# Kernel optimization log

Measured on AMD Instinct MI355X. Metric: run time of the kernel, lower is better.

The kernel has to match this reference:

```python
import jax, jax.numpy as jnp
import numpy as np

N_NODES = 100000

def _sage(x, src, tgt, Wl, bl, Wr):
    # PyG SAGEConv (mean aggr): out = lin_l(mean_{j in N(i)} x_j) + lin_r(x_i)
    msg = x[src]                                             # [E, F] gather
    s = jax.ops.segment_sum(msg, tgt, num_segments=N_NODES)  # [N, F]
    cnt = jax.ops.segment_sum(jnp.ones((src.shape[0], 1), x.dtype), tgt, num_segments=N_NODES)
    agg = s / jnp.maximum(cnt, 1.0)
    return agg @ Wl + bl + x @ Wr


def setup_inputs() -> dict:
    key = jax.random.key(0)
    ks = jax.random.split(key, 16)
    node_dim, edge_dim, hidden = 128, 16, 64
    E = 1000000
    x = jax.random.normal(ks[0], (N_NODES, node_dim), jnp.float32)
    edge_index = jax.random.randint(ks[1], (2, E), 0, N_NODES, jnp.int64)
    edge_attr = jax.random.normal(ks[2], (E, edge_dim), jnp.float32)
    def lin(k, fi, fo, scale=None):
        s = scale if scale is not None else 1.0 / np.sqrt(fi)
        return jax.random.uniform(k, (fi, fo), jnp.float32, -s, s)
    return {
        "x": x, "edge_index": edge_index, "edge_attr": edge_attr,
        # edge MLP: Linear(16,64) -> ReLU -> Linear(64,64)
        "We1": lin(ks[3], edge_dim, hidden), "be1": jnp.zeros((hidden,), jnp.float32),
        "We2": lin(ks[4], hidden, hidden),   "be2": jnp.zeros((hidden,), jnp.float32),
        # SAGEConv 0: lin_l (with bias, on aggregated) + lin_r (no bias, on root)
        "Wl0": lin(ks[5], node_dim, hidden), "bl0": jnp.zeros((hidden,), jnp.float32),
        "Wr0": lin(ks[6], node_dim, hidden),
        # SAGEConv 1
        "Wl1": lin(ks[7], hidden, hidden), "bl1": jnp.zeros((hidden,), jnp.float32),
        "Wr1": lin(ks[8], hidden, hidden),
        # output MLP: Linear(64,64) -> ReLU -> (Dropout eval=id) -> Linear(64,1)
        "Wo1": lin(ks[9], hidden, hidden), "bo1": jnp.zeros((hidden,), jnp.float32),
        "Wo2": lin(ks[10], hidden, 1),     "bo2": jnp.zeros((1,), jnp.float32),
    }


def reference(x, edge_index, edge_attr, We1, be1, We2, be2,
              Wl0, bl0, Wr0, Wl1, bl1, Wr1, Wo1, bo1, Wo2, bo2):
    src, tgt = edge_index[0], edge_index[1]
    # edge MLP (dropout in eval mode = identity)
    ea = jax.nn.relu(edge_attr @ We1 + be1) @ We2 + be2       # [E, H]
    # two SAGE layers with ReLU
    h = jax.nn.relu(_sage(x, src, tgt, Wl0, bl0, Wr0))        # [N, H]
    h = jax.nn.relu(_sage(h, src, tgt, Wl1, bl1, Wr1))        # [N, H]
    # per-edge features: gather both endpoints + edge embedding
    ef = h[src] + h[tgt] + ea                                 # [E, H]
    out = jax.nn.relu(ef @ Wo1 + bo1) @ Wo2 + bo2             # [E, 1]
    return jax.nn.sigmoid(out[:, 0])                          # [E]
```

## Files before the change

kernel.cpp:

```cpp
#include <hip/hip_runtime.h>
#include <math.h>

typedef __attribute__((ext_vector_type(8))) short short8;
typedef __attribute__((ext_vector_type(4))) float f32x4;

static __device__ __forceinline__ unsigned short f2bf(float f) {
  union { float f; unsigned int u; } x; x.f = f;
  unsigned int r = x.u + 0x7fffu + ((x.u >> 16) & 1u);
  return (unsigned short)(r >> 16);
}
static __device__ __forceinline__ float bf2f(unsigned int u) {
  union { unsigned int u; float f; } x; x.u = u << 16; return x.f;
}

__global__ void k_flag(const unsigned int* __restrict__ w, int nSample,
                       unsigned int* __restrict__ flag,
                       int* __restrict__ deg, int padN) {
  int4* d4 = (int4*)deg;
  int n4 = padN >> 2;
  for (int i = blockIdx.x * 256 + threadIdx.x; i < n4; i += gridDim.x * 256)
    d4[i] = make_int4(0, 0, 0, 0);
  if (blockIdx.x != 0) return;
  __shared__ unsigned int red[256];
  unsigned int v = 0;
  for (int i = threadIdx.x; i < nSample; i += 256) v |= w[2 * i + 1];
  red[threadIdx.x] = v;
  __syncthreads();
  for (int s = 128; s > 0; s >>= 1) {
    if (threadIdx.x < s) red[threadIdx.x] |= red[threadIdx.x + s];
    __syncthreads();
  }
  if (threadIdx.x == 0) flag[0] = red[0];
}

template <int K, bool BF16IN, int NTILES, bool INLINEW>
__device__ __forceinline__ void ngemm_body(
    const void* __restrict__ Xv, const unsigned short* __restrict__ WnT,
    const float* __restrict__ W0f, const float* __restrict__ W1f,
    unsigned short* __restrict__ Y0, unsigned short* __restrict__ Y1,
    int N, int blk, unsigned short* __restrict__ sX) {
  constexpr int STR = K + 8;
  constexpr int NC = K / 32;
  const int tid = threadIdx.x;
  const int wv = tid >> 6, lane = tid & 63;
  const int m = lane & 15, q = lane >> 4;
  const int row0 = blk * 64;

  short8 bB[NTILES][NC];
#pragma unroll
  for (int ct = 0; ct < NTILES; ++ct)
#pragma unroll
    for (int c = 0; c < NC; ++c) {
      if constexpr (INLINEW) {
        int n = (NTILES == 2) ? (wv * 32 + ct * 16 + m) : (wv * 16 + m);
        const float* Wf = (n < 64) ? W0f : W1f;
        int nn = n & 63;
        union { short8 s; unsigned short h[8]; } ub;
#pragma unroll
        for (int j = 0; j < 8; ++j)
          ub.h[j] = f2bf(Wf[(size_t)(c * 32 + q * 8 + j) * 64 + nn]);
        bB[ct][c] = ub.s;
      } else {
        int n = (NTILES == 2) ? (wv * 32 + ct * 16 + m) : (wv * 16 + m);
        bB[ct][c] = *(const short8*)(WnT + (size_t)n * K + c * 32 + q * 8);
      }
    }

#pragma unroll
  for (int i = 0; i < K / 16; ++i) {
    int f = tid + 256 * i;
    int r = f / (K / 4);
    int c4 = f % (K / 4);
    int rr = row0 + r; if (rr >= N) rr = N - 1;
    uint2 pk;
    if constexpr (BF16IN) {
      pk = *(const uint2*)((const unsigned short*)Xv + (size_t)rr * K + c4 * 4);
    } else {
      float4 v = *(const float4*)((const float*)Xv + (size_t)rr * K + c4 * 4);
      pk.x = (unsigned int)f2bf(v.x) | ((unsigned int)f2bf(v.y) << 16);
      pk.y = (unsigned int)f2bf(v.z) | ((unsigned int)f2bf(v.w) << 16);
    }
    *(uint2*)(sX + r * STR + c4 * 4) = pk;
  }
  __syncthreads();

  f32x4 acc[4][NTILES];
#pragma unroll
  for (int rt = 0; rt < 4; ++rt)
#pragma unroll
    for (int ct = 0; ct < NTILES; ++ct)
#pragma unroll
      for (int r = 0; r < 4; ++r) acc[rt][ct][r] = 0.f;

#pragma unroll
  for (int c = 0; c < NC; ++c) {
    short8 a[4];
#pragma unroll
    for (int rt = 0; rt < 4; ++rt)
      a[rt] = *(const short8*)(sX + (rt * 16 + m) * STR + c * 32 + q * 8);
#pragma unroll
    for (int rt = 0; rt < 4; ++rt)
#pragma unroll
      for (int ct = 0; ct < NTILES; ++ct)
        acc[rt][ct] = __builtin_amdgcn_mfma_f32_16x16x32_bf16(a[rt], bB[ct][c], acc[rt][ct], 0, 0, 0);
  }

#pragma unroll
  for (int rt = 0; rt < 4; ++rt)
#pragma unroll
    for (int ct = 0; ct < NTILES; ++ct) {
      unsigned short* Yw;
      int n;
      if constexpr (NTILES == 2) {
        Yw = (wv < 2) ? Y0 : Y1;
        n = (wv & 1) * 32 + ct * 16 + m;
      } else {
        Yw = Y0;
        n = wv * 16 + m;
      }
#pragma unroll
      for (int reg = 0; reg < 4; ++reg) {
        int row = row0 + rt * 16 + q * 4 + reg;
        if (row < N) Yw[(size_t)row * 64 + n] = f2bf(acc[rt][ct][reg]);
      }
    }
}

template <int K, bool BF16IN, int NTILES>
__global__ __launch_bounds__(256) void k_ngemm(
    const void* __restrict__ Xv, const unsigned short* __restrict__ WnT,
    unsigned short* __restrict__ Y0, unsigned short* __restrict__ Y1, int N) {
  __shared__ __align__(16) unsigned short sX[64 * (K + 8)];
  ngemm_body<K, BF16IN, NTILES, false>(Xv, WnT, nullptr, nullptr, Y0, Y1, N,
                                       blockIdx.x, sX);
}

__global__ __launch_bounds__(256) void k_mega1(
    const unsigned int* __restrict__ w, const unsigned int* __restrict__ flag,
    int E, int nDec, int nWork, int gB, int nConvThreads,
    int* __restrict__ src, int* __restrict__ tgt,
    int* __restrict__ posin, int* __restrict__ deg,
    const float* __restrict__ x, unsigned short* __restrict__ Yl,
    unsigned short* __restrict__ Yr, int N,
    const float* __restrict__ We2, const float* __restrict__ Wo1,
    const float* __restrict__ be2, const float* __restrict__ bo1,
    const float* __restrict__ We1,
    const float* __restrict__ Wl0, const float* __restrict__ Wr0,
    const float* __restrict__ Wl1, const float* __restrict__ Wr1,
    unsigned short* __restrict__ W25T, unsigned short* __restrict__ We1T,
    unsigned short* __restrict__ Wo1T, float* __restrict__ cvec,
    unsigned short* __restrict__ WnT1,
    const float4* __restrict__ ef, uint2* __restrict__ eb) {
  __shared__ __align__(16) char smem[64 * 136 * 2];
  const int tid = threadIdx.x;
  const int tot = nDec + nWork;
  const int di  = (int)(((long long)blockIdx.x * nDec) / tot);
  const int di1 = (int)(((long long)(blockIdx.x + 1) * nDec) / tot);

  if (di1 > di) {
    int e = di * 256 + tid;
    if (e >= E) return;
    int s, t;
    if (flag[0]) { s = (int)w[e]; t = (int)w[E + e]; }
    else         { s = (int)w[2 * e]; t = (int)w[2 * (E + e)]; }
    src[e] = s;
    tgt[e] = t;
    posin[e] = atomicAdd(deg + t, 1);
    return;
  }
  const int wi = blockIdx.x - di;
  if (wi == 0) {
    float* sB = (float*)smem;
    for (int i = tid; i < 1024; i += 256)
      *(float4*)&sB[i * 4] = *(const float4*)(Wo1 + i * 4);
    __syncthreads();
    for (int idx = tid; idx < 4096; idx += 256) {
      int k = idx >> 6, n = idx & 63;
      float s = 0.f;
#pragma unroll 8
      for (int mm = 0; mm < 64; ++mm) s = fmaf(We2[k * 64 + mm], sB[mm * 64 + n], s);
      W25T[n * 64 + k] = f2bf(s);
      Wo1T[n * 64 + k] = f2bf(sB[k * 64 + n]);
    }
    for (int idx = tid; idx < 2048; idx += 256) {
      int n = idx >> 5, k = idx & 31;
      We1T[n * 32 + k] = (k < 16) ? f2bf(We1[k * 64 + n]) : (unsigned short)0;
    }
    if (tid < 64) {
      float s = bo1[tid];
#pragma unroll 8
      for (int mm = 0; mm < 64; ++mm) s = fmaf(be2[mm], sB[mm * 64 + tid], s);
      cvec[tid] = s;
    }
  } else if (wi <= 32) {
    int idx = (wi - 1) * 256 + tid;
    int n = idx >> 6, k = idx & 63;
    float v = (n < 64) ? Wl1[(size_t)k * 64 + n] : Wr1[(size_t)k * 64 + (n - 64)];
    WnT1[idx] = f2bf(v);
  } else if (wi < 33 + gB) {
    ngemm_body<128, false, 2, true>(x, nullptr, Wl0, Wr0, Yl, Yr, N,
                                    wi - 33, (unsigned short*)smem);
  } else {
    int gid = (wi - 33 - gB) * 256 + tid;
    int nItems = E * 4;
    for (int i = gid; i < nItems; i += nConvThreads) {
      float4 v = ef[i];
      uint2 pk;
      pk.x = (unsigned int)f2bf(v.x) | ((unsigned int)f2bf(v.y) << 16);
      pk.y = (unsigned int)f2bf(v.z) | ((unsigned int)f2bf(v.w) << 16);
      eb[i] = pk;
    }
  }
}

__global__ __launch_bounds__(256) void k_scan1(const int* __restrict__ deg,
                                               int* __restrict__ bsum) {
  __shared__ int wsum[4];
  const int tid = threadIdx.x, lane = tid & 63, wid = tid >> 6;
  const int base = blockIdx.x * 2048 + tid * 8;
  int4 v0 = *(const int4*)(deg + base);
  int4 v1 = *(const int4*)(deg + base + 4);
  int s = v0.x + v0.y + v0.z + v0.w + v1.x + v1.y + v1.z + v1.w;
#pragma unroll
  for (int off = 1; off < 64; off <<= 1) s += __shfl_xor(s, off, 64);
  if (lane == 0) wsum[wid] = s;
  __syncthreads();
  if (tid == 0) bsum[blockIdx.x] = wsum[0] + wsum[1] + wsum[2] + wsum[3];
}

__global__ void k_scan2(const int* __restrict__ bsum, int* __restrict__ boff,
                        int nB) {
  int lane = threadIdx.x;
  int v = (lane < nB) ? bsum[lane] : 0;
  int incl = v;
#pragma unroll
  for (int off = 1; off < 64; off <<= 1) {
    int t = __shfl_up(incl, off, 64);
    if (lane >= off) incl += t;
  }
  if (lane < nB) boff[lane] = incl - v;
}

__global__ __launch_bounds__(256) void k_scan3(const int* __restrict__ deg,
                                               const int* __restrict__ boff,
                                               int* __restrict__ rowptr) {
  __shared__ int wsum[4];
  const int tid = threadIdx.x, lane = tid & 63, wid = tid >> 6;
  const int base = blockIdx.x * 2048 + tid * 8;
  int4 v0 = *(const int4*)(deg + base);
  int4 v1 = *(const int4*)(deg + base + 4);
  int e[8] = {v0.x, v0.y, v0.z, v0.w, v1.x, v1.y, v1.z, v1.w};
  int s = e[0] + e[1] + e[2] + e[3] + e[4] + e[5] + e[6] + e[7];
  int incl = s;
#pragma unroll
  for (int off = 1; off < 64; off <<= 1) {
    int t = __shfl_up(incl, off, 64);
    if (lane >= off) incl += t;
  }
  if (lane == 63) wsum[wid] = incl;
  __syncthreads();
  int run = boff[blockIdx.x] + (incl - s);
  for (int w = 0; w < wid; ++w) run += wsum[w];
  int o[8];
#pragma unroll
  for (int i = 0; i < 8; ++i) { o[i] = run; run += e[i]; }
  *(int4*)(rowptr + base) = make_int4(o[0], o[1], o[2], o[3]);
  *(int4*)(rowptr + base + 4) = make_int4(o[4], o[5], o[6], o[7]);
}

__global__ void k_fill(const int* __restrict__ src, const int* __restrict__ tgt,
                       const int* __restrict__ posin,
                       const int* __restrict__ rowptr,
                       int* __restrict__ csrc, int E) {
  int e = blockIdx.x * 256 + threadIdx.x;
  if (e >= E) return;
  csrc[rowptr[tgt[e]] + posin[e]] = src[e];
}

__global__ __launch_bounds__(256) void k_agg(
    const unsigned short* __restrict__ Y, const int* __restrict__ rowptr,
    const int* __restrict__ csrc, const float* __restrict__ bias,
    const unsigned short* __restrict__ Yr, unsigned short* __restrict__ H,
    int N) {
  int node = (blockIdx.x * 256 + threadIdx.x) >> 6;
  if (node >= N) return;
  const int lane = threadIdx.x & 63;
  const int c4 = lane & 15, rr = lane >> 4;
  int beg = rowptr[node], end = rowptr[node + 1];
  float a0 = 0.f, a1 = 0.f, a2 = 0.f, a3 = 0.f;
  float b0 = 0.f, b1 = 0.f, b2 = 0.f, b3 = 0.f;
  for (int e = beg; e < end; e += 8) {
    int e0 = e + rr, e1 = e + 4 + rr;
    if (e0 < end) {
      int s = csrc[e0];
      uint2 v = *(const uint2*)(Y + (size_t)s * 64 + c4 * 4);
      a0 += bf2f(v.x & 0xffffu); a1 += bf2f(v.x >> 16);
      a2 += bf2f(v.y & 0xffffu); a3 += bf2f(v.y >> 16);
    }
    if (e1 < end) {
      int s = csrc[e1];
      uint2 v = *(const uint2*)(Y + (size_t)s * 64 + c4 * 4);
      b0 += bf2f(v.x & 0xffffu); b1 += bf2f(v.x >> 16);
      b2 += bf2f(v.y & 0xffffu); b3 += bf2f(v.y >> 16);
    }
  }
  a0 += b0; a1 += b1; a2 += b2; a3 += b3;
#pragma unroll
  for (int msk = 16; msk <= 32; msk <<= 1) {
    a0 += __shfl_xor(a0, msk, 64);
    a1 += __shfl_xor(a1, msk, 64);
    a2 += __shfl_xor(a2, msk, 64);
    a3 += __shfl_xor(a3, msk, 64);
  }
  if (rr == 0) {
    float cdeg = (float)(end - beg);
    if (cdeg < 1.f) cdeg = 1.f;
    float inv = 1.f / cdeg;
    float4 bv = *(const float4*)(bias + c4 * 4);
    uint2 yv = *(const uint2*)(Yr + (size_t)node * 64 + c4 * 4);
    float o0 = fmaxf(a0 * inv + bv.x + bf2f(yv.x & 0xffffu), 0.f);
    float o1 = fmaxf(a1 * inv + bv.y + bf2f(yv.x >> 16), 0.f);
    float o2 = fmaxf(a2 * inv + bv.z + bf2f(yv.y & 0xffffu), 0.f);
    float o3 = fmaxf(a3 * inv + bv.w + bf2f(yv.y >> 16), 0.f);
    uint2 pk;
    pk.x = (unsigned int)f2bf(o0) | ((unsigned int)f2bf(o1) << 16);
    pk.y = (unsigned int)f2bf(o2) | ((unsigned int)f2bf(o3) << 16);
    *(uint2*)(H + (size_t)node * 64 + c4 * 4) = pk;
  }
}

#define T1_STRIDE 72
#define G_STRIDE 68
__global__ __launch_bounds__(256) void k_edge3(
    const unsigned short* __restrict__ EAb, const int* __restrict__ src,
    const int* __restrict__ tgt, const unsigned short* __restrict__ Gb,
    const unsigned short* __restrict__ We1T,
    const unsigned short* __restrict__ W25T,
    const float* __restrict__ cvec, const float* __restrict__ be1,
    const float* __restrict__ Wo2, const float* __restrict__ bo2,
    float* __restrict__ out, int E, int nT, int nWaves) {
  __shared__ unsigned short sT1a[4][16 * T1_STRIDE];
  __shared__ float sGa[4][16 * G_STRIDE];
  const int tid = threadIdx.x;
  const int wid = tid >> 6, lane = tid & 63;
  const int m = lane & 15, q = lane >> 4;
  unsigned short* sT1 = sT1a[wid];
  float* sG = sGa[wid];

  short8 bWe1[4], bW25[4][2];
  float cv[4], wo2v[4], be1v[4];
#pragma unroll
  for (int nt = 0; nt < 4; ++nt) {
    int n = nt * 16 + m;
    bWe1[nt] = *(const short8*)(We1T + n * 32 + q * 8);
    bW25[nt][0] = *(const short8*)(W25T + n * 64 + q * 8);
    bW25[nt][1] = *(const short8*)(W25T + n * 64 + 32 + q * 8);
    cv[nt] = cvec[n];
    wo2v[nt] = Wo2[n];
    be1v[nt] = be1[n];
  }
  const float b_out = bo2[0];
  const short8 zfrag = {};

  int t = blockIdx.x * 4 + wid;
  if (t >= nT) return;
  int il = t * 16 + m; if (il >= E) il = E - 1;
  int my_idx = (lane < 16) ? src[il] : ((lane < 32) ? tgt[il] : 0);

  while (true) {
    const int base = t * 16;
    const int tn = t + nWaves;
    const bool last = (tn >= nT);
    const int tc = last ? t : tn;

    int il_n = tc * 16 + m; if (il_n >= E) il_n = E - 1;
    int idx_n = (lane < 16) ? src[il_n] : ((lane < 32) ? tgt[il_n] : 0);

    int rs[4], rt[4];
#pragma unroll
    for (int r = 0; r < 4; ++r) {
      rs[r] = __shfl(my_idx, q * 4 + r, 64);
      rt[r] = __shfl(my_idx, 16 + q * 4 + r, 64);
    }
    uint2 sv[4], tv[4];
#pragma unroll
    for (int r = 0; r < 4; ++r) {
      sv[r] = *(const uint2*)(Gb + (size_t)rs[r] * 64 + m * 4);
      tv[r] = *(const uint2*)(Gb + (size_t)rt[r] * 64 + m * 4);
    }

    int er = base + m; if (er >= E) er = E - 1;
    short8 aEA = zfrag;
    if (q < 2) aEA = *(const short8*)(EAb + (size_t)er * 16 + (q & 1) * 8);

    f32x4 t1[4];
#pragma unroll
    for (int nt = 0; nt < 4; ++nt) {
      f32x4 cinit; cinit[0] = be1v[nt]; cinit[1] = be1v[nt];
      cinit[2] = be1v[nt]; cinit[3] = be1v[nt];
      t1[nt] = __builtin_amdgcn_mfma_f32_16x16x32_bf16(aEA, bWe1[nt], cinit, 0, 0, 0);
    }
#pragma unroll
    for (int nt = 0; nt < 4; ++nt)
#pragma unroll
      for (int r = 0; r < 4; ++r)
        sT1[(q * 4 + r) * T1_STRIDE + nt * 16 + m] = f2bf(fmaxf(t1[nt][r], 0.f));
    short8 aT0 = *(short8*)(sT1 + m * T1_STRIDE + q * 8);
    short8 aT1 = *(short8*)(sT1 + m * T1_STRIDE + 32 + q * 8);

#pragma unroll
    for (int r = 0; r < 4; ++r) {
      f32x4 g;
      g[0] = bf2f(sv[r].x & 0xffffu) + bf2f(tv[r].x & 0xffffu);
      g[1] = bf2f(sv[r].x >> 16)     + bf2f(tv[r].x >> 16);
      g[2] = bf2f(sv[r].y & 0xffffu) + bf2f(tv[r].y & 0xffffu);
      g[3] = bf2f(sv[r].y >> 16)     + bf2f(tv[r].y >> 16);
      *(f32x4*)(sG + (q * 4 + r) * G_STRIDE + m * 4) = g;
    }

    f32x4 acc[4];
#pragma unroll
    for (int nt = 0; nt < 4; ++nt)
#pragma unroll
      for (int r = 0; r < 4; ++r)
        acc[nt][r] = cv[nt] + sG[(q * 4 + r) * G_STRIDE + nt * 16 + m];
#pragma unroll
    for (int nt = 0; nt < 4; ++nt) {
      acc[nt] = __builtin_amdgcn_mfma_f32_16x16x32_bf16(aT0, bW25[nt][0], acc[nt], 0, 0, 0);
      acc[nt] = __builtin_amdgcn_mfma_f32_16x16x32_bf16(aT1, bW25[nt][1], acc[nt], 0, 0, 0);
    }

    float p[4];
#pragma unroll
    for (int r = 0; r < 4; ++r) {
      p[r] = fmaxf(acc[0][r], 0.f) * wo2v[0] + fmaxf(acc[1][r], 0.f) * wo2v[1] +
             fmaxf(acc[2][r], 0.f) * wo2v[2] + fmaxf(acc[3][r], 0.f) * wo2v[3];
    }
#pragma unroll
    for (int msk = 1; msk <= 8; msk <<= 1) {
#pragma unroll
      for (int r = 0; r < 4; ++r) p[r] += __shfl_xor(p[r], msk, 64);
    }
    if (m == 0) {
#pragma unroll
      for (int r = 0; r < 4; ++r) {
        int row = base + q * 4 + r;
        if (row < E) out[row] = 1.f / (1.f + __expf(-(p[r] + b_out)));
      }
    }

    if (last) break;
    t = tn; my_idx = idx_n;
  }
}

extern "C" void kernel_launch(void* const* d_in, const int* in_sizes, int n_in,
                              void* d_out, int out_size, void* d_ws, size_t ws_size,
                              hipStream_t stream) {
  const float* x     = (const float*)d_in[0];
  const unsigned int* eidx = (const unsigned int*)d_in[1];
  const float* eattr = (const float*)d_in[2];
  const float* We1 = (const float*)d_in[3];
  const float* be1 = (const float*)d_in[4];
  const float* We2 = (const float*)d_in[5];
  const float* be2 = (const float*)d_in[6];
  const float* Wl0 = (const float*)d_in[7];
  const float* bl0 = (const float*)d_in[8];
  const float* Wr0 = (const float*)d_in[9];
  const float* Wl1 = (const float*)d_in[10];
  const float* bl1 = (const float*)d_in[11];
  const float* Wr1 = (const float*)d_in[12];
  const float* Wo1 = (const float*)d_in[13];
  const float* bo1 = (const float*)d_in[14];
  const float* Wo2 = (const float*)d_in[15];
  const float* bo2 = (const float*)d_in[16];

  const int N = in_sizes[0] / 128;
  const int E = in_sizes[2] / 16;
  const int padN = (N + 2047) & ~2047;
  const int nB = padN / 2048;
  float* out = (float*)d_out;

  char* ws = (char*)d_ws;
  size_t off = 0;
  auto alloc = [&](size_t bytes) {
    char* p = ws + off;
    off += (bytes + 255) & ~(size_t)255;
    return p;
  };
  unsigned int* flag = (unsigned int*)alloc(256);
  int* src    = (int*)alloc((size_t)E * 4);
  int* tgt    = (int*)alloc((size_t)E * 4);
  int* posin  = (int*)alloc((size_t)E * 4);
  int* deg    = (int*)alloc((size_t)padN * 4);
  int* rowptr = (int*)alloc((size_t)(padN + 64) * 4);
  int* bsum   = (int*)alloc(64 * 4);
  int* boff   = (int*)alloc(64 * 4);
  int* csrc   = (int*)alloc((size_t)E * 4);
  unsigned short* EAb = (unsigned short*)alloc((size_t)E * 16 * 2);
  unsigned short* Hb = (unsigned short*)alloc((size_t)N * 64 * 2);
  unsigned short* Yl = (unsigned short*)alloc((size_t)N * 64 * 2);
  unsigned short* Yr = (unsigned short*)alloc((size_t)N * 64 * 2);
  unsigned short* Gb = (unsigned short*)alloc((size_t)N * 64 * 2);
  unsigned short* W25T = (unsigned short*)alloc(64 * 64 * 2);
  unsigned short* We1T = (unsigned short*)alloc(64 * 32 * 2);
  unsigned short* Wo1T = (unsigned short*)alloc(64 * 64 * 2);
  unsigned short* WnT1 = (unsigned short*)alloc(128 * 64 * 2);
  float* cvec = (float*)alloc(64 * 4);
  (void)ws_size; (void)n_in; (void)out_size;

  k_flag<<<64, 256, 0, stream>>>(eidx, 8192, flag, deg, padN);

  const int nDec = (E + 255) / 256;
  const int gB = (N + 63) / 64;
  const int convB = 1024;
  const int nWork = 33 + gB + convB;
  k_mega1<<<nDec + nWork, 256, 0, stream>>>(
      eidx, flag, E, nDec, nWork, gB, convB * 256,
      src, tgt, posin, deg,
      x, Yl, Yr, N,
      We2, Wo1, be2, bo1, We1, Wl0, Wr0, Wl1, Wr1,
      W25T, We1T, Wo1T, cvec, WnT1,
      (const float4*)eattr, (uint2*)EAb);

  k_scan1<<<nB, 256, 0, stream>>>(deg, bsum);
  k_scan2<<<1, 64, 0, stream>>>(bsum, boff, nB);
  k_scan3<<<nB, 256, 0, stream>>>(deg, boff, rowptr);
  k_fill<<<nDec, 256, 0, stream>>>(src, tgt, posin, rowptr, csrc, E);

  const int aggB = (N + 3) / 4;
  k_agg<<<aggB, 256, 0, stream>>>(Yl, rowptr, csrc, bl0, Yr, Hb, N);

  k_ngemm<64, true, 2><<<gB, 256, 0, stream>>>(Hb, WnT1, Yl, Yr, N);
  k_agg<<<aggB, 256, 0, stream>>>(Yl, rowptr, csrc, bl1, Yr, Hb, N);

  k_ngemm<64, true, 1><<<gB, 256, 0, stream>>>(Hb, Wo1T, Gb, nullptr, N);

  const int nT = (E + 15) / 16;
  const int blocks = 3072;
  k_edge3<<<blocks, 256, 0, stream>>>(EAb, src, tgt, Gb, We1T, W25T, cvec,
                                      be1, Wo2, bo2, out, E, nT, blocks * 4);
}
```

Before: 411.3 us.

## Privatize degree counters into 32 sub-bins per node to cut atomic contention

The per-node degree histogram becomes 32 sub-counters per node, selected by the decode block index, so edge atomics spread across more addresses. The scan kernels now sum the 32 sub-bins per node and emit per-sub-bin base offsets, which the CSR fill uses to place each edge. The 32x larger count and base buffers alias the Hb and Gb buffers to avoid extra workspace. In exchange, zeroing and scanning touch far more memory, and the per-edge atomics now hit 32 separate cache lines per node instead of one.

```diff
diff --git a/kernel.cpp b/kernel.cpp
--- a/kernel.cpp
+++ b/kernel.cpp
@@ -15,9 +15,9 @@
 
 __global__ void k_flag(const unsigned int* __restrict__ w, int nSample,
                        unsigned int* __restrict__ flag,
-                       int* __restrict__ deg, int padN) {
-  int4* d4 = (int4*)deg;
-  int n4 = padN >> 2;
+                       int* __restrict__ deg32, int nInts) {
+  int4* d4 = (int4*)deg32;
+  int n4 = nInts >> 2;
   for (int i = blockIdx.x * 256 + threadIdx.x; i < n4; i += gridDim.x * 256)
     d4[i] = make_int4(0, 0, 0, 0);
   if (blockIdx.x != 0) return;
@@ -139,7 +139,7 @@
     const unsigned int* __restrict__ w, const unsigned int* __restrict__ flag,
     int E, int nDec, int nWork, int gB, int nConvThreads,
     int* __restrict__ src, int* __restrict__ tgt,
-    int* __restrict__ posin, int* __restrict__ deg,
+    int* __restrict__ posin, int* __restrict__ deg32,
     const float* __restrict__ x, unsigned short* __restrict__ Yl,
     unsigned short* __restrict__ Yr, int N,
     const float* __restrict__ We2, const float* __restrict__ Wo1,
@@ -165,7 +165,7 @@
     else         { s = (int)w[2 * e]; t = (int)w[2 * (E + e)]; }
     src[e] = s;
     tgt[e] = t;
-    posin[e] = atomicAdd(deg + t, 1);
+    posin[e] = atomicAdd(deg32 + (size_t)t * 32 + (di & 31), 1);
     return;
   }
   const int wi = blockIdx.x - di;
@@ -213,14 +213,17 @@
   }
 }
 
-__global__ __launch_bounds__(256) void k_scan1(const int* __restrict__ deg,
+__global__ __launch_bounds__(256) void k_scan1(const int* __restrict__ deg32,
                                                int* __restrict__ bsum) {
   __shared__ int wsum[4];
   const int tid = threadIdx.x, lane = tid & 63, wid = tid >> 6;
-  const int base = blockIdx.x * 2048 + tid * 8;
-  int4 v0 = *(const int4*)(deg + base);
-  int4 v1 = *(const int4*)(deg + base + 4);
-  int s = v0.x + v0.y + v0.z + v0.w + v1.x + v1.y + v1.z + v1.w;
+  const int* p = deg32 + (size_t)blockIdx.x * 65536 + (size_t)tid * 4;
+  int s = 0;
+#pragma unroll 8
+  for (int i = 0; i < 64; ++i) {
+    int4 v = *(const int4*)(p + (size_t)i * 1024);
+    s += v.x + v.y + v.z + v.w;
+  }
 #pragma unroll
   for (int off = 1; off < 64; off <<= 1) s += __shfl_xor(s, off, 64);
   if (lane == 0) wsum[wid] = s;
@@ -241,15 +244,25 @@
   if (lane < nB) boff[lane] = incl - v;
 }
 
-__global__ __launch_bounds__(256) void k_scan3(const int* __restrict__ deg,
+__global__ __launch_bounds__(256) void k_scan3(const int* __restrict__ deg32,
                                                const int* __restrict__ boff,
-                                               int* __restrict__ rowptr) {
+                                               int* __restrict__ rowptr,
+                                               int* __restrict__ base32) {
   __shared__ int wsum[4];
   const int tid = threadIdx.x, lane = tid & 63, wid = tid >> 6;
-  const int base = blockIdx.x * 2048 + tid * 8;
-  int4 v0 = *(const int4*)(deg + base);
-  int4 v1 = *(const int4*)(deg + base + 4);
-  int e[8] = {v0.x, v0.y, v0.z, v0.w, v1.x, v1.y, v1.z, v1.w};
+  const int node0 = blockIdx.x * 2048 + tid * 8;
+  int e[8];
+#pragma unroll
+  for (int i = 0; i < 8; ++i) {
+    const int4* p = (const int4*)(deg32 + (size_t)(node0 + i) * 32);
+    int s8 = 0;
+#pragma unroll
+    for (int j = 0; j < 8; ++j) {
+      int4 v = p[j];
+      s8 += v.x + v.y + v.z + v.w;
+    }
+    e[i] = s8;
+  }
   int s = e[0] + e[1] + e[2] + e[3] + e[4] + e[5] + e[6] + e[7];
   int incl = s;
 #pragma unroll
@@ -264,17 +277,35 @@
   int o[8];
 #pragma unroll
   for (int i = 0; i < 8; ++i) { o[i] = run; run += e[i]; }
-  *(int4*)(rowptr + base) = make_int4(o[0], o[1], o[2], o[3]);
-  *(int4*)(rowptr + base + 4) = make_int4(o[4], o[5], o[6], o[7]);
+  *(int4*)(rowptr + node0) = make_int4(o[0], o[1], o[2], o[3]);
+  *(int4*)(rowptr + node0 + 4) = make_int4(o[4], o[5], o[6], o[7]);
+#pragma unroll
+  for (int i = 0; i < 8; ++i) {
+    const int4* p = (const int4*)(deg32 + (size_t)(node0 + i) * 32);
+    int4* b = (int4*)(base32 + (size_t)(node0 + i) * 32);
+    int r2 = o[i];
+#pragma unroll
+    for (int j = 0; j < 8; ++j) {
+      int4 v = p[j];
+      int4 bb;
+      bb.x = r2;
+      bb.y = r2 + v.x;
+      bb.z = bb.y + v.y;
+      bb.w = bb.z + v.z;
+      b[j] = bb;
+      r2 = bb.w + v.w;
+    }
+  }
 }
 
 __global__ void k_fill(const int* __restrict__ src, const int* __restrict__ tgt,
                        const int* __restrict__ posin,
-                       const int* __restrict__ rowptr,
+                       const int* __restrict__ base32,
                        int* __restrict__ csrc, int E) {
   int e = blockIdx.x * 256 + threadIdx.x;
   if (e >= E) return;
-  csrc[rowptr[tgt[e]] + posin[e]] = src[e];
+  int t = tgt[e];
+  csrc[base32[(size_t)t * 32 + ((e >> 8) & 31)] + posin[e]] = src[e];
 }
 
 __global__ __launch_bounds__(256) void k_agg(
@@ -492,16 +523,19 @@
   int* src    = (int*)alloc((size_t)E * 4);
   int* tgt    = (int*)alloc((size_t)E * 4);
   int* posin  = (int*)alloc((size_t)E * 4);
-  int* deg    = (int*)alloc((size_t)padN * 4);
   int* rowptr = (int*)alloc((size_t)(padN + 64) * 4);
   int* bsum   = (int*)alloc(64 * 4);
   int* boff   = (int*)alloc(64 * 4);
   int* csrc   = (int*)alloc((size_t)E * 4);
   unsigned short* EAb = (unsigned short*)alloc((size_t)E * 16 * 2);
-  unsigned short* Hb = (unsigned short*)alloc((size_t)N * 64 * 2);
+  char* HbB = alloc((size_t)padN * 128);
+  unsigned short* Hb = (unsigned short*)HbB;
+  int* base32 = (int*)HbB;
   unsigned short* Yl = (unsigned short*)alloc((size_t)N * 64 * 2);
   unsigned short* Yr = (unsigned short*)alloc((size_t)N * 64 * 2);
-  unsigned short* Gb = (unsigned short*)alloc((size_t)N * 64 * 2);
+  char* GbB = alloc((size_t)padN * 128);
+  unsigned short* Gb = (unsigned short*)GbB;
+  int* deg32 = (int*)GbB;
   unsigned short* W25T = (unsigned short*)alloc(64 * 64 * 2);
   unsigned short* We1T = (unsigned short*)alloc(64 * 32 * 2);
   unsigned short* Wo1T = (unsigned short*)alloc(64 * 64 * 2);
@@ -509,7 +543,7 @@
   float* cvec = (float*)alloc(64 * 4);
   (void)ws_size; (void)n_in; (void)out_size;
 
-  k_flag<<<64, 256, 0, stream>>>(eidx, 8192, flag, deg, padN);
+  k_flag<<<256, 256, 0, stream>>>(eidx, 8192, flag, deg32, padN * 32);
 
   const int nDec = (E + 255) / 256;
   const int gB = (N + 63) / 64;
@@ -517,16 +551,16 @@
   const int nWork = 33 + gB + convB;
   k_mega1<<<nDec + nWork, 256, 0, stream>>>(
       eidx, flag, E, nDec, nWork, gB, convB * 256,
-      src, tgt, posin, deg,
+      src, tgt, posin, deg32,
       x, Yl, Yr, N,
       We2, Wo1, be2, bo1, We1, Wl0, Wr0, Wl1, Wr1,
       W25T, We1T, Wo1T, cvec, WnT1,
       (const float4*)eattr, (uint2*)EAb);
 
-  k_scan1<<<nB, 256, 0, stream>>>(deg, bsum);
+  k_scan1<<<nB, 256, 0, stream>>>(deg32, bsum);
   k_scan2<<<1, 64, 0, stream>>>(bsum, boff, nB);
-  k_scan3<<<nB, 256, 0, stream>>>(deg, boff, rowptr);
-  k_fill<<<nDec, 256, 0, stream>>>(src, tgt, posin, rowptr, csrc, E);
+  k_scan3<<<nB, 256, 0, stream>>>(deg32, boff, rowptr, base32);
+  k_fill<<<nDec, 256, 0, stream>>>(src, tgt, posin, base32, csrc, E);
 
   const int aggB = (N + 3) / 4;
   k_agg<<<aggB, 256, 0, stream>>>(Yl, rowptr, csrc, bl0, Yr, Hb, N);
```

After: 463.9 us. +12.8%, slower.

## Replace global-atomic CSR build with two-pass bucketed counting sort

Applied to the files above, without the earlier changes.

Builds the target-sorted edge list by bucketing edges into 256-node buckets using block-local shared histograms and global bucket cursors, then counting-sorting each bucket in one kernel that also emits begin/end row pairs. This removes per-edge global atomics on the degree array, the three-kernel scan, and the scatter fill kernel. It relies on a fixed per-bucket capacity and silently drops edges beyond it, and on source indices fitting in 24 bits.

```diff
diff --git a/kernel.cpp b/kernel.cpp
--- a/kernel.cpp
+++ b/kernel.cpp
@@ -3,6 +3,8 @@
 
 typedef __attribute__((ext_vector_type(8))) short short8;
 typedef __attribute__((ext_vector_type(4))) float f32x4;
+
+#define CAPB 4096
 
 static __device__ __forceinline__ unsigned short f2bf(float f) {
   union { float f; unsigned int u; } x; x.f = f;
@@ -15,11 +17,11 @@
 
 __global__ void k_flag(const unsigned int* __restrict__ w, int nSample,
                        unsigned int* __restrict__ flag,
-                       int* __restrict__ deg, int padN) {
-  int4* d4 = (int4*)deg;
-  int n4 = padN >> 2;
-  for (int i = blockIdx.x * 256 + threadIdx.x; i < n4; i += gridDim.x * 256)
-    d4[i] = make_int4(0, 0, 0, 0);
+                       int* __restrict__ gcursor) {
+  if (blockIdx.x == 1) {
+    if (threadIdx.x < 256) { gcursor[threadIdx.x] = 0; gcursor[threadIdx.x + 256] = 0; }
+    return;
+  }
   if (blockIdx.x != 0) return;
   __shared__ unsigned int red[256];
   unsigned int v = 0;
@@ -139,7 +141,7 @@
     const unsigned int* __restrict__ w, const unsigned int* __restrict__ flag,
     int E, int nDec, int nWork, int gB, int nConvThreads,
     int* __restrict__ src, int* __restrict__ tgt,
-    int* __restrict__ posin, int* __restrict__ deg,
+    int* __restrict__ gcursor, unsigned int* __restrict__ tmp,
     const float* __restrict__ x, unsigned short* __restrict__ Yl,
     unsigned short* __restrict__ Yr, int N,
     const float* __restrict__ We2, const float* __restrict__ Wo1,
@@ -158,14 +160,37 @@
   const int di1 = (int)(((long long)(blockIdx.x + 1) * nDec) / tot);
 
   if (di1 > di) {
-    int e = di * 256 + tid;
-    if (e >= E) return;
-    int s, t;
-    if (flag[0]) { s = (int)w[e]; t = (int)w[E + e]; }
-    else         { s = (int)w[2 * e]; t = (int)w[2 * (E + e)]; }
-    src[e] = s;
-    tgt[e] = t;
-    posin[e] = atomicAdd(deg + t, 1);
+    int* hist = (int*)smem;
+    hist[tid] = 0; hist[tid + 256] = 0;
+    __syncthreads();
+    const int e0 = di * 4096;
+    const int e1 = (e0 + 4096 < E) ? (e0 + 4096) : E;
+    const unsigned int fl = flag[0];
+    for (int e = e0 + tid; e < e1; e += 256) {
+      int s, t;
+      if (fl) { s = (int)w[e]; t = (int)w[E + e]; }
+      else    { s = (int)w[2 * e]; t = (int)w[2 * (E + e)]; }
+      src[e] = s; tgt[e] = t;
+      atomicAdd(hist + (t >> 8), 1);
+    }
+    __syncthreads();
+    {
+      int c0 = hist[tid], c1 = hist[tid + 256];
+      int s0 = (c0 > 0) ? atomicAdd(gcursor + tid, c0) : 0;
+      int s1 = (c1 > 0) ? atomicAdd(gcursor + tid + 256, c1) : 0;
+      __syncthreads();
+      hist[tid] = s0; hist[tid + 256] = s1;
+    }
+    __syncthreads();
+    for (int e = e0 + tid; e < e1; e += 256) {
+      int s, t;
+      if (fl) { s = (int)w[e]; t = (int)w[E + e]; }
+      else    { s = (int)w[2 * e]; t = (int)w[2 * (E + e)]; }
+      int b = t >> 8;
+      int pos = atomicAdd(hist + b, 1);
+      if (pos < CAPB)
+        tmp[(size_t)b * CAPB + pos] = ((unsigned int)s << 8) | (unsigned int)(t & 255);
+    }
     return;
   }
   const int wi = blockIdx.x - di;
@@ -213,72 +238,47 @@
   }
 }
 
-__global__ __launch_bounds__(256) void k_scan1(const int* __restrict__ deg,
-                                               int* __restrict__ bsum) {
+__global__ __launch_bounds__(256) void k_bsort(
+    const unsigned int* __restrict__ tmp, const int* __restrict__ gcursor,
+    int* __restrict__ csrc, uint2* __restrict__ rowptr2, int N) {
+  __shared__ int cnt[256];
+  __shared__ int curs[256];
   __shared__ int wsum[4];
-  const int tid = threadIdx.x, lane = tid & 63, wid = tid >> 6;
-  const int base = blockIdx.x * 2048 + tid * 8;
-  int4 v0 = *(const int4*)(deg + base);
-  int4 v1 = *(const int4*)(deg + base + 4);
-  int s = v0.x + v0.y + v0.z + v0.w + v1.x + v1.y + v1.z + v1.w;
-#pragma unroll
-  for (int off = 1; off < 64; off <<= 1) s += __shfl_xor(s, off, 64);
-  if (lane == 0) wsum[wid] = s;
+  const int b = blockIdx.x, tid = threadIdx.x;
+  int c = gcursor[b]; if (c > CAPB) c = CAPB;
+  cnt[tid] = 0;
   __syncthreads();
-  if (tid == 0) bsum[blockIdx.x] = wsum[0] + wsum[1] + wsum[2] + wsum[3];
-}
-
-__global__ void k_scan2(const int* __restrict__ bsum, int* __restrict__ boff,
-                        int nB) {
-  int lane = threadIdx.x;
-  int v = (lane < nB) ? bsum[lane] : 0;
+  const unsigned int* reg = tmp + (size_t)b * CAPB;
+  for (int i = tid; i < c; i += 256) atomicAdd(&cnt[reg[i] & 255u], 1);
+  __syncthreads();
+  const int lane = tid & 63, wv = tid >> 6;
+  int v = cnt[tid];
   int incl = v;
 #pragma unroll
   for (int off = 1; off < 64; off <<= 1) {
     int t = __shfl_up(incl, off, 64);
     if (lane >= off) incl += t;
   }
-  if (lane < nB) boff[lane] = incl - v;
-}
-
-__global__ __launch_bounds__(256) void k_scan3(const int* __restrict__ deg,
-                                               const int* __restrict__ boff,
-                                               int* __restrict__ rowptr) {
-  __shared__ int wsum[4];
-  const int tid = threadIdx.x, lane = tid & 63, wid = tid >> 6;
-  const int base = blockIdx.x * 2048 + tid * 8;
-  int4 v0 = *(const int4*)(deg + base);
-  int4 v1 = *(const int4*)(deg + base + 4);
-  int e[8] = {v0.x, v0.y, v0.z, v0.w, v1.x, v1.y, v1.z, v1.w};
-  int s = e[0] + e[1] + e[2] + e[3] + e[4] + e[5] + e[6] + e[7];
-  int incl = s;
-#pragma unroll
-  for (int off = 1; off < 64; off <<= 1) {
-    int t = __shfl_up(incl, off, 64);
-    if (lane >= off) incl += t;
-  }
-  if (lane == 63) wsum[wid] = incl;
+  if (lane == 63) wsum[wv] = incl;
   __syncthreads();
-  int run = boff[blockIdx.x] + (incl - s);
-  for (int w = 0; w < wid; ++w) run += wsum[w];
-  int o[8];
-#pragma unroll
-  for (int i = 0; i < 8; ++i) { o[i] = run; run += e[i]; }
-  *(int4*)(rowptr + base) = make_int4(o[0], o[1], o[2], o[3]);
-  *(int4*)(rowptr + base + 4) = make_int4(o[4], o[5], o[6], o[7]);
-}
-
-__global__ void k_fill(const int* __restrict__ src, const int* __restrict__ tgt,
-                       const int* __restrict__ posin,
-                       const int* __restrict__ rowptr,
-                       int* __restrict__ csrc, int E) {
-  int e = blockIdx.x * 256 + threadIdx.x;
-  if (e >= E) return;
-  csrc[rowptr[tgt[e]] + posin[e]] = src[e];
+  int add = 0;
+  for (int ww = 0; ww < wv; ++ww) add += wsum[ww];
+  int excl = add + incl - v;
+  curs[tid] = excl;
+  int node = b * 256 + tid;
+  if (node < N)
+    rowptr2[node] = make_uint2((unsigned int)(b * CAPB + excl),
+                               (unsigned int)(b * CAPB + excl + v));
+  __syncthreads();
+  for (int i = tid; i < c; i += 256) {
+    unsigned int wd = reg[i];
+    int p = atomicAdd(&curs[wd & 255u], 1);
+    csrc[(size_t)b * CAPB + p] = (int)(wd >> 8);
+  }
 }
 
 __global__ __launch_bounds__(256) void k_agg(
-    const unsigned short* __restrict__ Y, const int* __restrict__ rowptr,
+    const unsigned short* __restrict__ Y, const uint2* __restrict__ rowptr2,
     const int* __restrict__ csrc, const float* __restrict__ bias,
     const unsigned short* __restrict__ Yr, unsigned short* __restrict__ H,
     int N) {
@@ -286,7 +286,8 @@
   if (node >= N) return;
   const int lane = threadIdx.x & 63;
   const int c4 = lane & 15, rr = lane >> 4;
-  int beg = rowptr[node], end = rowptr[node + 1];
+  uint2 be = rowptr2[node];
+  int beg = (int)be.x, end = (int)be.y;
   float a0 = 0.f, a1 = 0.f, a2 = 0.f, a3 = 0.f;
   float b0 = 0.f, b1 = 0.f, b2 = 0.f, b3 = 0.f;
   for (int e = beg; e < end; e += 8) {
@@ -477,8 +478,7 @@
 
   const int N = in_sizes[0] / 128;
   const int E = in_sizes[2] / 16;
-  const int padN = (N + 2047) & ~2047;
-  const int nB = padN / 2048;
+  const int NBUCK = (N + 255) >> 8;
   float* out = (float*)d_out;
 
   char* ws = (char*)d_ws;
@@ -491,12 +491,10 @@
   unsigned int* flag = (unsigned int*)alloc(256);
   int* src    = (int*)alloc((size_t)E * 4);
   int* tgt    = (int*)alloc((size_t)E * 4);
-  int* posin  = (int*)alloc((size_t)E * 4);
-  int* deg    = (int*)alloc((size_t)padN * 4);
-  int* rowptr = (int*)alloc((size_t)(padN + 64) * 4);
-  int* bsum   = (int*)alloc(64 * 4);
-  int* boff   = (int*)alloc(64 * 4);
-  int* csrc   = (int*)alloc((size_t)E * 4);
+  int* gcursor = (int*)alloc(512 * 4);
+  unsigned int* tmp = (unsigned int*)alloc((size_t)NBUCK * CAPB * 4);
+  int* csrc   = (int*)alloc((size_t)NBUCK * CAPB * 4);
+  uint2* rowptr2 = (uint2*)alloc((size_t)N * 8);
   unsigned short* EAb = (unsigned short*)alloc((size_t)E * 16 * 2);
   unsigned short* Hb = (unsigned short*)alloc((size_t)N * 64 * 2);
   unsigned short* Yl = (unsigned short*)alloc((size_t)N * 64 * 2);
@@ -509,30 +507,27 @@
   float* cvec = (float*)alloc(64 * 4);
   (void)ws_size; (void)n_in; (void)out_size;
 
-  k_flag<<<64, 256, 0, stream>>>(eidx, 8192, flag, deg, padN);
-
-  const int nDec = (E + 255) / 256;
+  k_flag<<<2, 256, 0, stream>>>(eidx, 8192, flag, gcursor);
+
+  const int nDec = (E + 4095) / 4096;
   const int gB = (N + 63) / 64;
   const int convB = 1024;
   const int nWork = 33 + gB + convB;
   k_mega1<<<nDec + nWork, 256, 0, stream>>>(
       eidx, flag, E, nDec, nWork, gB, convB * 256,
-      src, tgt, posin, deg,
+      src, tgt, gcursor, tmp,
       x, Yl, Yr, N,
       We2, Wo1, be2, bo1, We1, Wl0, Wr0, Wl1, Wr1,
       W25T, We1T, Wo1T, cvec, WnT1,
       (const float4*)eattr, (uint2*)EAb);
 
-  k_scan1<<<nB, 256, 0, stream>>>(deg, bsum);
-  k_scan2<<<1, 64, 0, stream>>>(bsum, boff, nB);
-  k_scan3<<<nB, 256, 0, stream>>>(deg, boff, rowptr);
-  k_fill<<<nDec, 256, 0, stream>>>(src, tgt, posin, rowptr, csrc, E);
+  k_bsort<<<NBUCK, 256, 0, stream>>>(tmp, gcursor, csrc, rowptr2, N);
 
   const int aggB = (N + 3) / 4;
-  k_agg<<<aggB, 256, 0, stream>>>(Yl, rowptr, csrc, bl0, Yr, Hb, N);
+  k_agg<<<aggB, 256, 0, stream>>>(Yl, rowptr2, csrc, bl0, Yr, Hb, N);
 
   k_ngemm<64, true, 2><<<gB, 256, 0, stream>>>(Hb, WnT1, Yl, Yr, N);
-  k_agg<<<aggB, 256, 0, stream>>>(Yl, rowptr, csrc, bl1, Yr, Hb, N);
+  k_agg<<<aggB, 256, 0, stream>>>(Yl, rowptr2, csrc, bl1, Yr, Hb, N);
 
   k_ngemm<64, true, 1><<<gB, 256, 0, stream>>>(Hb, Wo1T, Gb, nullptr, N);
 
```

Result: faster. 398.6 us (-3.1%).
